# Kernel tuning notes

Hardware: AMD Instinct MI355X
Metric: run time of the kernel (lower is better)

Reference implementation:

```python
import jax, jax.numpy as jnp
import numpy as np

N = 50000
E = 1600000
IN_DIM = 32
EDGE_DIM = 32
HID = 64
OUT = 32


def setup_inputs() -> dict:
    key = jax.random.key(0)
    ks = jax.random.split(key, 12)
    x = jax.random.normal(ks[0], (N, IN_DIM), dtype=jnp.float32)
    edge_index = jax.random.randint(ks[1], (2, E), 0, N, dtype=jnp.int64)
    edge_attr = jax.random.normal(ks[2], (E, EDGE_DIM), dtype=jnp.float32)
    # MLP params: Linear(64->64), Linear(64->128), Linear(128->64), Linear(64->32)
    def lin(k, fan_in, fan_out):
        lim = 1.0 / np.sqrt(fan_in)
        kw, kb = jax.random.split(k)
        W = jax.random.uniform(kw, (fan_in, fan_out), minval=-lim, maxval=lim, dtype=jnp.float32)
        b = jax.random.uniform(kb, (fan_out,), minval=-lim, maxval=lim, dtype=jnp.float32)
        return W, b
    W1, b1 = lin(ks[3], IN_DIM + EDGE_DIM, HID)
    W2, b2 = lin(ks[4], HID, 2 * HID)
    W3, b3 = lin(ks[5], 2 * HID, HID)
    W4, b4 = lin(ks[6], HID, OUT)
    return {"x": x, "edge_index": edge_index, "edge_attr": edge_attr,
            "W1": W1, "b1": b1, "W2": W2, "b2": b2,
            "W3": W3, "b3": b3, "W4": W4, "b4": b4}


def reference(x, edge_index, edge_attr, W1, b1, W2, b2, W3, b3, W4, b4):
    # PyG MessagePassing (source_to_target): x_i = x[edge_index[1]] (target),
    # messages aggregated (mean) at target nodes edge_index[1].
    dst = edge_index[1]
    x_i = x[dst]                                   # [E, IN_DIM] gather
    m = jnp.concatenate([x_i, edge_attr], axis=-1)  # [E, 64]
    # 4-layer MLP with ReLU (dropout = identity at inference)
    m = jax.nn.relu(m @ W1 + b1)                   # [E, 64]
    m = jax.nn.relu(m @ W2 + b2)                   # [E, 128]
    m = jax.nn.relu(m @ W3 + b3)                   # [E, 64]
    m = jax.nn.relu(m @ W4 + b4)                   # [E, 32]
    # mean scatter to target nodes
    sums = jax.ops.segment_sum(m, dst, num_segments=N)          # [N, 32]
    cnt = jax.ops.segment_sum(jnp.ones((E,), m.dtype), dst, num_segments=N)
    out = sums / jnp.maximum(cnt, 1.0)[:, None]
    return out
```

## Files before the change

kernel.cpp:

```cpp
#include <hip/hip_runtime.h>
#include <hip/hip_bf16.h>

typedef __attribute__((ext_vector_type(8))) unsigned short u16x8;
typedef __attribute__((ext_vector_type(8))) __bf16 bf16x8;
typedef __attribute__((ext_vector_type(4))) float f32x4;

__device__ __forceinline__ unsigned pack_bf2(float lo, float hi) {
  unsigned a = __float_as_uint(lo) + 0x8000u;
  unsigned b = __float_as_uint(hi) + 0x8000u;
  return __builtin_amdgcn_perm(b, a, 0x07060302);
}

__device__ __forceinline__ unsigned short f2bf(float f) {
  unsigned u = __float_as_uint(f);
  return (unsigned short)((u + 0x7fffu + ((u >> 16) & 1u)) >> 16);
}

__device__ __forceinline__ int aswz(int row, int feat, int stride) {
  return row * stride + (((feat >> 3) ^ (row & 7)) << 4) + (feat & 7) * 2;
}

__global__ void prep_weights(const float* __restrict__ W1, const float* __restrict__ W2,
                             const float* __restrict__ W3, const float* __restrict__ W4,
                             unsigned short* __restrict__ wt) {
  int i = blockIdx.x * 256 + threadIdx.x;
  if (i >= 22528) return;
  float v; int n, k, K, base;
  if (i < 4096)       { n = i >> 6, k = i & 63;  K = 64;  base = 0;     v = W1[k * 64 + n]; }
  else if (i < 12288) { int j = i - 4096;  n = j >> 6, k = j & 63;  K = 64;  base = 4096;  v = W2[k * 128 + n]; }
  else if (i < 20480) { int j = i - 12288; n = j >> 7, k = j & 127; K = 128; base = 12288; v = W3[k * 64 + n]; }
  else                { int j = i - 20480; n = j >> 6, k = j & 63;  K = 64;  base = 20480; v = W4[k * 32 + n]; }
  int o = base + n * K + ((((k >> 3) ^ (n & 7)) << 3) + (k & 7));
  wt[o] = f2bf(v);
}

__global__ void hist_kernel(const int* __restrict__ ei, int* __restrict__ histI, int E) {
  int e = blockIdx.x * 256 + threadIdx.x;
  if (e < E) atomicAdd(&histI[ei[E + e]], 1);
}

__global__ void scan_blocks(const int* __restrict__ histI, int* __restrict__ row_start,
                            int* __restrict__ blockSums, int N) {
  __shared__ int wsum[4];
  const int lane = threadIdx.x & 63, w = threadIdx.x >> 6;
  const int i0 = blockIdx.x * 2048 + threadIdx.x * 8;
  int v[8];
#pragma unroll
  for (int j = 0; j < 8; ++j) { int i = i0 + j; v[j] = (i < N) ? histI[i] : 0; }
  int s = 0;
#pragma unroll
  for (int j = 0; j < 8; ++j) { int t = v[j]; v[j] = s; s += t; }
  int ss = s;
#pragma unroll
  for (int d = 1; d < 64; d <<= 1) { int t = __shfl_up(ss, d, 64); if (lane >= d) ss += t; }
  if (lane == 63) wsum[w] = ss;
  __syncthreads();
  int wOff = 0;
#pragma unroll
  for (int k = 0; k < 4; ++k) if (k < w) wOff += wsum[k];
  const int tOff = wOff + (ss - s);
#pragma unroll
  for (int j = 0; j < 8; ++j) { int i = i0 + j; if (i < N) row_start[i] = tOff + v[j]; }
  if (threadIdx.x == 255) blockSums[blockIdx.x] = wOff + ss;
}

__global__ void scan_tops(int* __restrict__ blockSums, int nb) {
  const int lane = threadIdx.x;
  int v = (lane < nb) ? blockSums[lane] : 0;
  int s = v;
#pragma unroll
  for (int d = 1; d < 64; d <<= 1) { int t = __shfl_up(s, d, 64); if (lane >= d) s += t; }
  if (lane < nb) blockSums[lane] = s - v;
}

__global__ void scan_add(int* __restrict__ row_start, const int* __restrict__ blockSums, int N) {
  int i = blockIdx.x * 256 + threadIdx.x;
  if (i < N) row_start[i] += blockSums[i >> 11];
}

__global__ void fill_kernel(const int* __restrict__ ei, const int* __restrict__ row_start,
                            int* __restrict__ wcnt, int2* __restrict__ edlist, int E) {
  int e = blockIdx.x * 256 + threadIdx.x;
  if (e >= E) return;
  int d = ei[E + e];
  int slot = atomicAdd(&wcnt[d], 1);
  edlist[row_start[d] + slot] = make_int2(e, d);
}

template <int MT, int KS, int SS, int DS>
__device__ __forceinline__ void mlp_layer(const unsigned char* src, unsigned char* dst,
                                          const unsigned char* wl, const float* biasL, int lane) {
  const int edge = lane & 15, g = lane >> 4;
  asm volatile("s_waitcnt lgkmcnt(0)" ::: "memory");
  u16x8 bfrag[KS];
#pragma unroll
  for (int ks = 0; ks < KS; ++ks)
    bfrag[ks] = *(const u16x8*)(src + aswz(edge, ks * 32 + g * 8, SS));
#pragma unroll
  for (int mt = 0; mt < MT; ++mt) {
    const int n = mt * 16 + edge;
    u16x8 af[KS];
#pragma unroll
    for (int ks = 0; ks < KS; ++ks)
      af[ks] = *(const u16x8*)(wl + n * (KS * 64) + (((ks * 4 + g) ^ (edge & 7)) << 4));
    const float4 bv = *(const float4*)(biasL + mt * 16 + g * 4);
    f32x4 acc = {bv.x, bv.y, bv.z, bv.w};
    __builtin_amdgcn_s_setprio(1);
#pragma unroll
    for (int ks = 0; ks < KS; ++ks)
      acc = __builtin_amdgcn_mfma_f32_16x16x32_bf16(
          __builtin_bit_cast(bf16x8, af[ks]), __builtin_bit_cast(bf16x8, bfrag[ks]),
          acc, 0, 0, 0);
    __builtin_amdgcn_s_setprio(0);
    const int fb = mt * 16 + g * 4;
    uint2 q;
    q.x = pack_bf2(fmaxf(acc[0], 0.f), fmaxf(acc[1], 0.f));
    q.y = pack_bf2(fmaxf(acc[2], 0.f), fmaxf(acc[3], 0.f));
    *(uint2*)(dst + aswz(edge, fb, DS)) = q;
  }
}

__device__ __forceinline__ void load_tile(int ebase, int E, const int2* __restrict__ edlist,
                                          const float* __restrict__ x, const float* __restrict__ ea,
                                          int lane, float4& xa, float4& xb, float4& ya, float4& yb,
                                          int& dstA) {
  const int el = ebase + (lane >> 2);
  const int part = lane & 3;
  xa = make_float4(0.f, 0.f, 0.f, 0.f); xb = xa; ya = xa; yb = xa;
  if (el < E) {
    const int2 ed = edlist[el];
    const float4* xp = (const float4*)(x + (size_t)ed.y * 32 + part * 8);
    xa = xp[0]; xb = xp[1];
    const float4* ep = (const float4*)(ea + (size_t)ed.x * 32 + part * 8);
    ya = ep[0]; yb = ep[1];
  }
  const int pos = ebase + (lane & 15);
  dstA = (pos < E) ? edlist[pos].y : -1;
}

#define BIAS_OFF   45056
#define ACT_OFF    46208

__global__ __launch_bounds__(1024, 4)
void gnn_main(const float* __restrict__ x, const int2* __restrict__ edlist,
              const float* __restrict__ ea, const unsigned short* __restrict__ wt,
              const float* __restrict__ b1, const float* __restrict__ b2,
              const float* __restrict__ b3, const float* __restrict__ b4,
              float* __restrict__ out, int E, int numTiles) {
  __shared__ __align__(16) unsigned char lds[ACT_OFF + 16 * 6144];
  {
    const u16x8* gw = (const u16x8*)wt;
    u16x8* lw = (u16x8*)lds;
    for (int i = threadIdx.x; i < 2816; i += 1024) lw[i] = gw[i];
    float* biasW = (float*)(lds + BIAS_OFF);
    for (int i = threadIdx.x; i < 288; i += 1024) {
      float v;
      if (i < 64) v = b1[i];
      else if (i < 192) v = b2[i - 64];
      else if (i < 256) v = b3[i - 192];
      else v = b4[i - 256];
      biasW[i] = v;
    }
  }
  __syncthreads();

  const int lane = threadIdx.x & 63, wid = threadIdx.x >> 6;
  const int edge = lane & 15, g = lane >> 4;
  const float* biasLds = (const float*)(lds + BIAS_OFF);
  unsigned char* buf0 = lds + ACT_OFF + wid * 6144;
  unsigned char* buf1 = buf0 + 4096;
  const unsigned char* wl1 = lds;
  const unsigned char* wl2 = lds + 8192;
  const unsigned char* wl3 = lds + 24576;
  const unsigned char* wl4 = lds + 40960;

  const int wgl = blockIdx.x * 16 + wid;
  const int wstride = gridDim.x * 16;

  float4 xa, xb, ya, yb; int dstA = -1;
  if (wgl < numTiles) load_tile(wgl * 16, E, edlist, x, ea, lane, xa, xb, ya, yb, dstA);

  for (int tile = wgl; tile < numTiles; tile += wstride) {
    uint4 hx, he;
    hx.x = pack_bf2(xa.x, xa.y); hx.y = pack_bf2(xa.z, xa.w);
    hx.z = pack_bf2(xb.x, xb.y); hx.w = pack_bf2(xb.z, xb.w);
    he.x = pack_bf2(ya.x, ya.y); he.y = pack_bf2(ya.z, ya.w);
    he.z = pack_bf2(yb.x, yb.y); he.w = pack_bf2(yb.z, yb.w);
    const int e2 = lane >> 2, part = lane & 3;
    *(uint4*)(buf0 + aswz(e2, part * 8, 256)) = hx;
    *(uint4*)(buf0 + aswz(e2, 32 + part * 8, 256)) = he;

    const int curDst = dstA;

    const int nt = tile + wstride;
    float4 nxa, nxb, nya, nyb; int ndst = -1;
    if (nt < numTiles) load_tile(nt * 16, E, edlist, x, ea, lane, nxa, nxb, nya, nyb, ndst);
    else { nxa = make_float4(0,0,0,0); nxb = nxa; nya = nxa; nyb = nxa; }

    mlp_layer<4, 2, 256, 128>(buf0, buf1, wl1, biasLds + 0,   lane);
    mlp_layer<8, 2, 128, 256>(buf1, buf0, wl2, biasLds + 64,  lane);
    mlp_layer<4, 4, 256, 128>(buf0, buf1, wl3, biasLds + 192, lane);

    asm volatile("s_waitcnt lgkmcnt(0)" ::: "memory");
    u16x8 bf4[2];
#pragma unroll
    for (int ks = 0; ks < 2; ++ks)
      bf4[ks] = *(const u16x8*)(buf1 + aswz(edge, ks * 32 + g * 8, 128));
    float vals[8];
#pragma unroll
    for (int mt = 0; mt < 2; ++mt) {
      const int n = mt * 16 + edge;
      u16x8 af[2];
#pragma unroll
      for (int ks = 0; ks < 2; ++ks)
        af[ks] = *(const u16x8*)(wl4 + n * 128 + (((ks * 4 + g) ^ (edge & 7)) << 4));
      const float4 bv = *(const float4*)(biasLds + 256 + mt * 16 + g * 4);
      f32x4 acc = {bv.x, bv.y, bv.z, bv.w};
      __builtin_amdgcn_s_setprio(1);
#pragma unroll
      for (int ks = 0; ks < 2; ++ks)
        acc = __builtin_amdgcn_mfma_f32_16x16x32_bf16(
            __builtin_bit_cast(bf16x8, af[ks]), __builtin_bit_cast(bf16x8, bf4[ks]),
            acc, 0, 0, 0);
      __builtin_amdgcn_s_setprio(0);
#pragma unroll
      for (int r = 0; r < 4; ++r) vals[mt * 4 + r] = fmaxf(acc[r], 0.f);
    }

    const int li = edge;
    const int prev = __shfl_up(curDst, 1, 16);
    const bool is_head = (li == 0) || (prev != curDst);
    const unsigned long long hb = __ballot(is_head);
    const unsigned gm = (unsigned)((hb >> (g * 16)) & 0xFFFFu);
    const unsigned below = gm & ((1u << li) | ((1u << li) - 1u));
    const int dist = li - (31 - __clz(below));
#pragma unroll
    for (int d = 1; d < 16; d <<= 1) {
#pragma unroll
      for (int t = 0; t < 8; ++t) {
        const float tv = __shfl_up(vals[t], d, 16);
        if (dist >= d) vals[t] += tv;
      }
    }
    const bool is_end = (li == 15) || ((gm >> (li + 1)) & 1u);
    if (is_end && curDst >= 0) {
      float* op = out + (size_t)curDst * 32 + g * 4;
#pragma unroll
      for (int t = 0; t < 4; ++t) unsafeAtomicAdd(op + t, vals[t]);
#pragma unroll
      for (int t = 0; t < 4; ++t) unsafeAtomicAdd(op + 16 + t, vals[4 + t]);
    }

    xa = nxa; xb = nxb; ya = nya; yb = nyb; dstA = ndst;
  }
}

__global__ void div_kernel(float* __restrict__ out, const int* __restrict__ histI, int total) {
  int i = blockIdx.x * 256 + threadIdx.x;
  if (i < total) out[i] = out[i] / fmaxf((float)histI[i >> 5], 1.0f);
}

extern "C" void kernel_launch(void* const* d_in, const int* in_sizes, int n_in,
                              void* d_out, int out_size, void* d_ws, size_t ws_size,
                              hipStream_t stream) {
  const float* x  = (const float*)d_in[0];
  const int*   ei = (const int*)d_in[1];
  const float* ea = (const float*)d_in[2];
  const float* W1 = (const float*)d_in[3];
  const float* b1 = (const float*)d_in[4];
  const float* W2 = (const float*)d_in[5];
  const float* b2 = (const float*)d_in[6];
  const float* W3 = (const float*)d_in[7];
  const float* b3 = (const float*)d_in[8];
  const float* W4 = (const float*)d_in[9];
  const float* b4 = (const float*)d_in[10];
  const int N = in_sizes[0] / 32;
  const int E = in_sizes[1] / 2;
  float* out = (float*)d_out;

  char* ws = (char*)d_ws;
  size_t off = 0;
  auto alloc = [&](size_t bytes) { size_t o = off; off += (bytes + 255) & ~(size_t)255; return o; };
  int* histI      = (int*)(ws + alloc((size_t)N * 4));
  int* wcnt       = (int*)(ws + alloc((size_t)N * 4));
  int* row_start  = (int*)(ws + alloc((size_t)(N + 1) * 4));
  int* blockSums  = (int*)(ws + alloc(64 * 4));
  int2* edlist    = (int2*)(ws + alloc((size_t)E * 8));
  unsigned short* wt = (unsigned short*)(ws + alloc(22528 * 2));

  hipMemsetAsync(d_out, 0, (size_t)out_size * sizeof(float), stream);
  hipMemsetAsync(histI, 0, (size_t)N * 4, stream);
  hipMemsetAsync(wcnt, 0, (size_t)N * 4, stream);

  prep_weights<<<(22528 + 255) / 256, 256, 0, stream>>>(W1, W2, W3, W4, wt);
  hist_kernel<<<(E + 255) / 256, 256, 0, stream>>>(ei, histI, E);
  const int nb = (N + 2047) / 2048;
  scan_blocks<<<nb, 256, 0, stream>>>(histI, row_start, blockSums, N);
  scan_tops<<<1, 64, 0, stream>>>(blockSums, nb);
  scan_add<<<(N + 255) / 256, 256, 0, stream>>>(row_start, blockSums, N);
  fill_kernel<<<(E + 255) / 256, 256, 0, stream>>>(ei, row_start, wcnt, edlist, E);

  const int numTiles = (E + 15) / 16;
  gnn_main<<<256, 1024, 0, stream>>>(x, edlist, ea, wt, b1, b2, b3, b4, out, E, numTiles);
  const int total = N * 32;
  div_kernel<<<(total + 255) / 256, 256, 0, stream>>>(out, histI, total);
}
```

Baseline: 334.1 us.

## Fuse CSR build into one grid-barrier kernel and use atomic-free node-partitioned mean

Replaces the chain of prep, histogram, multi-stage scan and fill kernels (plus memsets and the divide kernel) with a single persistent kernel that uses software grid barriers. The main kernel now splits work by node ranges found through binary search on row_start, so each destination is owned by one wavefront. Segment sums carry across tiles and are written once, already divided by the count, instead of using atomic adds followed by a separate division pass. This cuts launch overhead and atomic traffic, but depends on all 256 blocks being co-resident for the barrier and adds more complex carry logic. The main grid also grows from 256 to 512 blocks.

```diff
diff --git a/kernel.cpp b/kernel.cpp
--- a/kernel.cpp
+++ b/kernel.cpp
@@ -4,6 +4,8 @@
 typedef __attribute__((ext_vector_type(8))) unsigned short u16x8;
 typedef __attribute__((ext_vector_type(8))) __bf16 bf16x8;
 typedef __attribute__((ext_vector_type(4))) float f32x4;
+
+#define CSR_NB 256
 
 __device__ __forceinline__ unsigned pack_bf2(float lo, float hi) {
   unsigned a = __float_as_uint(lo) + 0x8000u;
@@ -20,71 +22,107 @@
   return row * stride + (((feat >> 3) ^ (row & 7)) << 4) + (feat & 7) * 2;
 }
 
-__global__ void prep_weights(const float* __restrict__ W1, const float* __restrict__ W2,
-                             const float* __restrict__ W3, const float* __restrict__ W4,
-                             unsigned short* __restrict__ wt) {
-  int i = blockIdx.x * 256 + threadIdx.x;
-  if (i >= 22528) return;
-  float v; int n, k, K, base;
-  if (i < 4096)       { n = i >> 6, k = i & 63;  K = 64;  base = 0;     v = W1[k * 64 + n]; }
-  else if (i < 12288) { int j = i - 4096;  n = j >> 6, k = j & 63;  K = 64;  base = 4096;  v = W2[k * 128 + n]; }
-  else if (i < 20480) { int j = i - 12288; n = j >> 7, k = j & 127; K = 128; base = 12288; v = W3[k * 64 + n]; }
-  else                { int j = i - 20480; n = j >> 6, k = j & 63;  K = 64;  base = 20480; v = W4[k * 32 + n]; }
-  int o = base + n * K + ((((k >> 3) ^ (n & 7)) << 3) + (k & 7));
-  wt[o] = f2bf(v);
-}
-
-__global__ void hist_kernel(const int* __restrict__ ei, int* __restrict__ histI, int E) {
-  int e = blockIdx.x * 256 + threadIdx.x;
-  if (e < E) atomicAdd(&histI[ei[E + e]], 1);
-}
-
-__global__ void scan_blocks(const int* __restrict__ histI, int* __restrict__ row_start,
-                            int* __restrict__ blockSums, int N) {
+__device__ __forceinline__ void gbar(int* bar, int id) {
+  __threadfence();
+  __syncthreads();
+  if (threadIdx.x == 0) {
+    __hip_atomic_fetch_add(&bar[id], 1, __ATOMIC_ACQ_REL, __HIP_MEMORY_SCOPE_AGENT);
+    while (__hip_atomic_load(&bar[id], __ATOMIC_ACQUIRE, __HIP_MEMORY_SCOPE_AGENT) < CSR_NB)
+      __builtin_amdgcn_s_sleep(2);
+  }
+  __syncthreads();
+}
+
+__global__ __launch_bounds__(256)
+void csr_build(const float* __restrict__ W1, const float* __restrict__ W2,
+               const float* __restrict__ W3, const float* __restrict__ W4,
+               unsigned short* __restrict__ wt, const int* __restrict__ ei,
+               int* __restrict__ histI, int* __restrict__ row_start,
+               int* __restrict__ blockSums, int* __restrict__ wcnt,
+               int2* __restrict__ edlist, float* __restrict__ out,
+               int* __restrict__ bar, int E, int N) {
+  const int tid = blockIdx.x * 256 + threadIdx.x;
+  const int lane = threadIdx.x & 63, w = threadIdx.x >> 6;
+  const int NTH = CSR_NB * 256;
   __shared__ int wsum[4];
-  const int lane = threadIdx.x & 63, w = threadIdx.x >> 6;
-  const int i0 = blockIdx.x * 2048 + threadIdx.x * 8;
-  int v[8];
-#pragma unroll
-  for (int j = 0; j < 8; ++j) { int i = i0 + j; v[j] = (i < N) ? histI[i] : 0; }
-  int s = 0;
-#pragma unroll
-  for (int j = 0; j < 8; ++j) { int t = v[j]; v[j] = s; s += t; }
-  int ss = s;
-#pragma unroll
-  for (int d = 1; d < 64; d <<= 1) { int t = __shfl_up(ss, d, 64); if (lane >= d) ss += t; }
-  if (lane == 63) wsum[w] = ss;
+
+  if (tid < 22528) {
+    float v; int n, k, K, base;
+    if (tid < 4096)       { n = tid >> 6, k = tid & 63;  K = 64;  base = 0;     v = W1[k * 64 + n]; }
+    else if (tid < 12288) { int j = tid - 4096;  n = j >> 6, k = j & 63;  K = 64;  base = 4096;  v = W2[k * 128 + n]; }
+    else if (tid < 20480) { int j = tid - 12288; n = j >> 7, k = j & 127; K = 128; base = 12288; v = W3[k * 64 + n]; }
+    else                  { int j = tid - 20480; n = j >> 6, k = j & 63;  K = 64;  base = 20480; v = W4[k * 32 + n]; }
+    int o = base + n * K + ((((k >> 3) ^ (n & 7)) << 3) + (k & 7));
+    wt[o] = f2bf(v);
+  }
+  const int Ntot4 = N * 8;
+  for (int i = tid; i < Ntot4; i += NTH)
+    ((float4*)out)[i] = make_float4(0.f, 0.f, 0.f, 0.f);
+  for (int e0 = tid * 4; e0 < E; e0 += NTH * 4) {
+    if (e0 + 3 < E) {
+      const int4 d4 = *(const int4*)(ei + E + e0);
+      atomicAdd(&histI[d4.x], 1); atomicAdd(&histI[d4.y], 1);
+      atomicAdd(&histI[d4.z], 1); atomicAdd(&histI[d4.w], 1);
+    } else {
+      for (int e = e0; e < E; ++e) atomicAdd(&histI[ei[E + e]], 1);
+    }
+  }
+  gbar(bar, 0);
+
+  const int i = tid;
+  const int v = (i < N) ? histI[i] : 0;
+  int s = v;
+#pragma unroll
+  for (int d = 1; d < 64; d <<= 1) { int t = __shfl_up(s, d, 64); if (lane >= d) s += t; }
+  if (lane == 63) wsum[w] = s;
   __syncthreads();
   int wOff = 0;
 #pragma unroll
   for (int k = 0; k < 4; ++k) if (k < w) wOff += wsum[k];
-  const int tOff = wOff + (ss - s);
-#pragma unroll
-  for (int j = 0; j < 8; ++j) { int i = i0 + j; if (i < N) row_start[i] = tOff + v[j]; }
-  if (threadIdx.x == 255) blockSums[blockIdx.x] = wOff + ss;
-}
-
-__global__ void scan_tops(int* __restrict__ blockSums, int nb) {
-  const int lane = threadIdx.x;
-  int v = (lane < nb) ? blockSums[lane] : 0;
-  int s = v;
-#pragma unroll
-  for (int d = 1; d < 64; d <<= 1) { int t = __shfl_up(s, d, 64); if (lane >= d) s += t; }
-  if (lane < nb) blockSums[lane] = s - v;
-}
-
-__global__ void scan_add(int* __restrict__ row_start, const int* __restrict__ blockSums, int N) {
-  int i = blockIdx.x * 256 + threadIdx.x;
-  if (i < N) row_start[i] += blockSums[i >> 11];
-}
-
-__global__ void fill_kernel(const int* __restrict__ ei, const int* __restrict__ row_start,
-                            int* __restrict__ wcnt, int2* __restrict__ edlist, int E) {
-  int e = blockIdx.x * 256 + threadIdx.x;
-  if (e >= E) return;
-  int d = ei[E + e];
-  int slot = atomicAdd(&wcnt[d], 1);
-  edlist[row_start[d] + slot] = make_int2(e, d);
+  const int lexcl = wOff + (s - v);
+  if (threadIdx.x == 0) {
+    int bt = wsum[0] + wsum[1] + wsum[2] + wsum[3];
+    blockSums[blockIdx.x] = bt;
+  }
+  gbar(bar, 1);
+
+  if (blockIdx.x == 0 && threadIdx.x < 64) {
+    int run = 0;
+    for (int c = 0; c < 4; ++c) {
+      const int idx = c * 64 + lane;
+      const int bv = blockSums[idx];
+      int bs = bv;
+#pragma unroll
+      for (int d = 1; d < 64; d <<= 1) { int t = __shfl_up(bs, d, 64); if (lane >= d) bs += t; }
+      const int ctot = __shfl(bs, 63, 64);
+      blockSums[idx] = run + bs - bv;
+      run += ctot;
+    }
+    if (lane == 0) row_start[N] = E;
+  }
+  gbar(bar, 2);
+
+  if (i < N) row_start[i] = blockSums[blockIdx.x] + lexcl;
+  gbar(bar, 3);
+
+  for (int e0 = tid * 4; e0 < E; e0 += NTH * 4) {
+    if (e0 + 3 < E) {
+      const int4 d4 = *(const int4*)(ei + E + e0);
+      const int dv[4] = {d4.x, d4.y, d4.z, d4.w};
+#pragma unroll
+      for (int j = 0; j < 4; ++j) {
+        const int d = dv[j];
+        const int slot = atomicAdd(&wcnt[d], 1);
+        edlist[row_start[d] + slot] = make_int2(e0 + j, d);
+      }
+    } else {
+      for (int e = e0; e < E; ++e) {
+        const int d = ei[E + e];
+        const int slot = atomicAdd(&wcnt[d], 1);
+        edlist[row_start[d] + slot] = make_int2(e, d);
+      }
+    }
+  }
 }
 
 template <int MT, int KS, int SS, int DS>
@@ -120,33 +158,40 @@
   }
 }
 
-__device__ __forceinline__ void load_tile(int ebase, int E, const int2* __restrict__ edlist,
+__device__ __forceinline__ void load_tile(int pbase, int pend, const int2* __restrict__ edlist,
                                           const float* __restrict__ x, const float* __restrict__ ea,
                                           int lane, float4& xa, float4& xb, float4& ya, float4& yb,
                                           int& dstA) {
-  const int el = ebase + (lane >> 2);
+  const int el = pbase + (lane >> 2);
   const int part = lane & 3;
   xa = make_float4(0.f, 0.f, 0.f, 0.f); xb = xa; ya = xa; yb = xa;
-  if (el < E) {
+  if (el < pend) {
     const int2 ed = edlist[el];
     const float4* xp = (const float4*)(x + (size_t)ed.y * 32 + part * 8);
     xa = xp[0]; xb = xp[1];
     const float4* ep = (const float4*)(ea + (size_t)ed.x * 32 + part * 8);
     ya = ep[0]; yb = ep[1];
   }
-  const int pos = ebase + (lane & 15);
-  dstA = (pos < E) ? edlist[pos].y : -1;
-}
-
-#define BIAS_OFF   45056
-#define ACT_OFF    46208
+  const int pos = pbase + (lane & 15);
+  dstA = (pos < pend) ? edlist[pos].y : -1;
+}
+
+__device__ __forceinline__ int lbound(const int* __restrict__ rs, int N, long tgt) {
+  int lo = 0, hi = N;
+  while (lo < hi) { int mid = (lo + hi) >> 1; if ((long)rs[mid] < tgt) lo = mid + 1; else hi = mid; }
+  return lo;
+}
+
+#define BIAS_OFF 45056
+#define ACT_OFF  46208
 
 __global__ __launch_bounds__(1024, 4)
 void gnn_main(const float* __restrict__ x, const int2* __restrict__ edlist,
               const float* __restrict__ ea, const unsigned short* __restrict__ wt,
+              const int* __restrict__ row_start,
               const float* __restrict__ b1, const float* __restrict__ b2,
               const float* __restrict__ b3, const float* __restrict__ b4,
-              float* __restrict__ out, int E, int numTiles) {
+              float* __restrict__ out, int E, int N) {
   __shared__ __align__(16) unsigned char lds[ACT_OFF + 16 * 6144];
   {
     const u16x8* gw = (const u16x8*)wt;
@@ -165,7 +210,7 @@
   __syncthreads();
 
   const int lane = threadIdx.x & 63, wid = threadIdx.x >> 6;
-  const int edge = lane & 15, g = lane >> 4;
+  const int li = lane & 15, g = lane >> 4;
   const float* biasLds = (const float*)(lds + BIAS_OFF);
   unsigned char* buf0 = lds + ACT_OFF + wid * 6144;
   unsigned char* buf1 = buf0 + 4096;
@@ -175,12 +220,21 @@
   const unsigned char* wl4 = lds + 40960;
 
   const int wgl = blockIdx.x * 16 + wid;
-  const int wstride = gridDim.x * 16;
+  const int W = gridDim.x * 16;
+  const int n0 = lbound(row_start, N, (long)wgl * E / W);
+  const int n1 = lbound(row_start, N, (long)(wgl + 1) * E / W);
+  const int pstart = row_start[n0];
+  const int pend = row_start[n1];
 
   float4 xa, xb, ya, yb; int dstA = -1;
-  if (wgl < numTiles) load_tile(wgl * 16, E, edlist, x, ea, lane, xa, xb, ya, yb, dstA);
-
-  for (int tile = wgl; tile < numTiles; tile += wstride) {
+  if (pstart < pend) load_tile(pstart, pend, edlist, x, ea, lane, xa, xb, ya, yb, dstA);
+
+  float carry[8];
+#pragma unroll
+  for (int t = 0; t < 8; ++t) carry[t] = 0.f;
+  int cDst = -1, cCnt = 0;
+
+  for (int pbase = pstart; pbase < pend; pbase += 16) {
     uint4 hx, he;
     hx.x = pack_bf2(xa.x, xa.y); hx.y = pack_bf2(xa.z, xa.w);
     hx.z = pack_bf2(xb.x, xb.y); hx.w = pack_bf2(xb.z, xb.w);
@@ -192,9 +246,9 @@
 
     const int curDst = dstA;
 
-    const int nt = tile + wstride;
-    float4 nxa, nxb, nya, nyb; int ndst = -1;
-    if (nt < numTiles) load_tile(nt * 16, E, edlist, x, ea, lane, nxa, nxb, nya, nyb, ndst);
+    const int np = pbase + 16;
+    float4 nxa, nxb, nya, nyb; int nd = -1;
+    if (np < pend) load_tile(np, pend, edlist, x, ea, lane, nxa, nxb, nya, nyb, nd);
     else { nxa = make_float4(0,0,0,0); nxb = nxa; nya = nxa; nyb = nxa; }
 
     mlp_layer<4, 2, 256, 128>(buf0, buf1, wl1, biasLds + 0,   lane);
@@ -205,15 +259,15 @@
     u16x8 bf4[2];
 #pragma unroll
     for (int ks = 0; ks < 2; ++ks)
-      bf4[ks] = *(const u16x8*)(buf1 + aswz(edge, ks * 32 + g * 8, 128));
+      bf4[ks] = *(const u16x8*)(buf1 + aswz(li, ks * 32 + g * 8, 128));
     float vals[8];
 #pragma unroll
     for (int mt = 0; mt < 2; ++mt) {
-      const int n = mt * 16 + edge;
+      const int n = mt * 16 + li;
       u16x8 af[2];
 #pragma unroll
       for (int ks = 0; ks < 2; ++ks)
-        af[ks] = *(const u16x8*)(wl4 + n * 128 + (((ks * 4 + g) ^ (edge & 7)) << 4));
+        af[ks] = *(const u16x8*)(wl4 + n * 128 + (((ks * 4 + g) ^ (li & 7)) << 4));
       const float4 bv = *(const float4*)(biasLds + 256 + mt * 16 + g * 4);
       f32x4 acc = {bv.x, bv.y, bv.z, bv.w};
       __builtin_amdgcn_s_setprio(1);
@@ -227,37 +281,97 @@
       for (int r = 0; r < 4; ++r) vals[mt * 4 + r] = fmaxf(acc[r], 0.f);
     }
 
-    const int li = edge;
-    const int prev = __shfl_up(curDst, 1, 16);
-    const bool is_head = (li == 0) || (prev != curDst);
-    const unsigned long long hb = __ballot(is_head);
-    const unsigned gm = (unsigned)((hb >> (g * 16)) & 0xFFFFu);
-    const unsigned below = gm & ((1u << li) | ((1u << li) - 1u));
-    const int dist = li - (31 - __clz(below));
-#pragma unroll
-    for (int d = 1; d < 16; d <<= 1) {
+    if (__all(curDst == cDst)) {
+#pragma unroll
+      for (int t = 0; t < 8; ++t) carry[t] += vals[t];
+      cCnt += 16;
+    } else {
+      const int prev = __shfl_up(curDst, 1, 16);
+      const bool is_head = (li == 0) || (prev != curDst);
+      const unsigned long long hb = __ballot(is_head);
+      const unsigned gm = (unsigned)((hb >> (g * 16)) & 0xFFFFu);
+      const unsigned below = gm & ((1u << li) | ((1u << li) - 1u));
+      const int dist = li - (31 - __clz(below));
+
+      float ctot[8];
 #pragma unroll
       for (int t = 0; t < 8; ++t) {
-        const float tv = __shfl_up(vals[t], d, 16);
-        if (dist >= d) vals[t] += tv;
-      }
-    }
-    const bool is_end = (li == 15) || ((gm >> (li + 1)) & 1u);
-    if (is_end && curDst >= 0) {
-      float* op = out + (size_t)curDst * 32 + g * 4;
-#pragma unroll
-      for (int t = 0; t < 4; ++t) unsafeAtomicAdd(op + t, vals[t]);
-#pragma unroll
-      for (int t = 0; t < 4; ++t) unsafeAtomicAdd(op + 16 + t, vals[4 + t]);
-    }
-
-    xa = nxa; xb = nxb; ya = nya; yb = nyb; dstA = ndst;
-  }
-}
-
-__global__ void div_kernel(float* __restrict__ out, const int* __restrict__ histI, int total) {
-  int i = blockIdx.x * 256 + threadIdx.x;
-  if (i < total) out[i] = out[i] / fmaxf((float)histI[i >> 5], 1.0f);
+        float c = carry[t];
+#pragma unroll
+        for (int d = 1; d < 16; d <<= 1) c += __shfl_xor(c, d, 16);
+        ctot[t] = c;
+      }
+
+      const int dst0 = __shfl(curDst, lane & 48, 64);
+      if (cDst >= 0 && dst0 != cDst && li == 0) {
+        const float inv = 1.0f / (float)cCnt;
+        float4 o0 = {ctot[0] * inv, ctot[1] * inv, ctot[2] * inv, ctot[3] * inv};
+        float4 o1 = {ctot[4] * inv, ctot[5] * inv, ctot[6] * inv, ctot[7] * inv};
+        *(float4*)(out + (size_t)cDst * 32 + g * 4) = o0;
+        *(float4*)(out + (size_t)cDst * 32 + 16 + g * 4) = o1;
+      }
+
+#pragma unroll
+      for (int d = 1; d < 16; d <<= 1) {
+#pragma unroll
+        for (int t = 0; t < 8; ++t) {
+          const float tv = __shfl_up(vals[t], d, 16);
+          if (dist >= d) vals[t] += tv;
+        }
+      }
+
+      const int ndst0 = __shfl(nd, lane & 48, 64);
+      const bool is_end = (li == 15) || ((gm >> (li + 1)) & 1u);
+      const bool complete = (li < 15) || (curDst != ndst0);
+      const bool firstAdd = (dist == li) && (curDst == cDst) && (cDst >= 0);
+      if (is_end && curDst >= 0 && complete) {
+        const int cnt = dist + 1 + (firstAdd ? cCnt : 0);
+        const float inv = 1.0f / (float)cnt;
+        float tot[8];
+#pragma unroll
+        for (int t = 0; t < 8; ++t) tot[t] = (vals[t] + (firstAdd ? ctot[t] : 0.f)) * inv;
+        float4 o0 = {tot[0], tot[1], tot[2], tot[3]};
+        float4 o1 = {tot[4], tot[5], tot[6], tot[7]};
+        *(float4*)(out + (size_t)curDst * 32 + g * 4) = o0;
+        *(float4*)(out + (size_t)curDst * 32 + 16 + g * 4) = o1;
+      }
+
+      const int dst15 = __shfl(curDst, lane | 15, 64);
+      const int d15 = __shfl(dist, lane | 15, 64);
+      const bool inc15 = (dst15 >= 0) && (dst15 == ndst0);
+      if (inc15) {
+#pragma unroll
+        for (int t = 0; t < 8; ++t)
+          carry[t] = (li == 15) ? (vals[t] + (firstAdd ? ctot[t] : 0.f)) : 0.f;
+        cCnt = d15 + 1 + ((d15 == 15 && dst15 == cDst) ? cCnt : 0);
+        cDst = dst15;
+      } else {
+#pragma unroll
+        for (int t = 0; t < 8; ++t) carry[t] = 0.f;
+        cCnt = 0; cDst = -1;
+      }
+    }
+
+    xa = nxa; xb = nxb; ya = nya; yb = nyb; dstA = nd;
+  }
+
+  if (cDst >= 0) {
+    float ctot[8];
+#pragma unroll
+    for (int t = 0; t < 8; ++t) {
+      float c = carry[t];
+#pragma unroll
+      for (int d = 1; d < 16; d <<= 1) c += __shfl_xor(c, d, 16);
+      ctot[t] = c;
+    }
+    if (li == 0) {
+      const float inv = 1.0f / (float)cCnt;
+      float4 o0 = {ctot[0] * inv, ctot[1] * inv, ctot[2] * inv, ctot[3] * inv};
+      float4 o1 = {ctot[4] * inv, ctot[5] * inv, ctot[6] * inv, ctot[7] * inv};
+      *(float4*)(out + (size_t)cDst * 32 + g * 4) = o0;
+      *(float4*)(out + (size_t)cDst * 32 + 16 + g * 4) = o1;
+    }
+  }
 }
 
 extern "C" void kernel_launch(void* const* d_in, const int* in_sizes, int n_in,
@@ -281,27 +395,21 @@
   char* ws = (char*)d_ws;
   size_t off = 0;
   auto alloc = [&](size_t bytes) { size_t o = off; off += (bytes + 255) & ~(size_t)255; return o; };
-  int* histI      = (int*)(ws + alloc((size_t)N * 4));
-  int* wcnt       = (int*)(ws + alloc((size_t)N * 4));
+  size_t bar_off  = alloc(256);
+  size_t hist_off = alloc((size_t)N * 4);
+  size_t wcnt_off = alloc((size_t)N * 4);
+  int* bar        = (int*)(ws + bar_off);
+  int* histI      = (int*)(ws + hist_off);
+  int* wcnt       = (int*)(ws + wcnt_off);
   int* row_start  = (int*)(ws + alloc((size_t)(N + 1) * 4));
-  int* blockSums  = (int*)(ws + alloc(64 * 4));
+  int* blockSums  = (int*)(ws + alloc(256 * 4));
   int2* edlist    = (int2*)(ws + alloc((size_t)E * 8));
   unsigned short* wt = (unsigned short*)(ws + alloc(22528 * 2));
 
-  hipMemsetAsync(d_out, 0, (size_t)out_size * sizeof(float), stream);
-  hipMemsetAsync(histI, 0, (size_t)N * 4, stream);
-  hipMemsetAsync(wcnt, 0, (size_t)N * 4, stream);
-
-  prep_weights<<<(22528 + 255) / 256, 256, 0, stream>>>(W1, W2, W3, W4, wt);
-  hist_kernel<<<(E + 255) / 256, 256, 0, stream>>>(ei, histI, E);
-  const int nb = (N + 2047) / 2048;
-  scan_blocks<<<nb, 256, 0, stream>>>(histI, row_start, blockSums, N);
-  scan_tops<<<1, 64, 0, stream>>>(blockSums, nb);
-  scan_add<<<(N + 255) / 256, 256, 0, stream>>>(row_start, blockSums, N);
-  fill_kernel<<<(E + 255) / 256, 256, 0, stream>>>(ei, row_start, wcnt, edlist, E);
-
-  const int numTiles = (E + 15) / 16;
-  gnn_main<<<256, 1024, 0, stream>>>(x, edlist, ea, wt, b1, b2, b3, b4, out, E, numTiles);
-  const int total = N * 32;
-  div_kernel<<<(total + 255) / 256, 256, 0, stream>>>(out, histI, total);
-}
+  hipMemsetAsync(ws, 0, wcnt_off + (size_t)N * 4, stream);
+
+  csr_build<<<CSR_NB, 256, 0, stream>>>(W1, W2, W3, W4, wt, ei, histI, row_start,
+                                        blockSums, wcnt, edlist, out, bar, E, N);
+  gnn_main<<<512, 1024, 0, stream>>>(x, edlist, ea, wt, row_start,
+                                     b1, b2, b3, b4, out, E, N);
+}
```

Result: slower. 450.4 us (+34.8%).

## Fuse preprocessing launches, partition atomics by XCD, fold mean division into scatter

Applied to the files above, without the earlier changes.

Merges weight prep with the histogram, and folds the top-level scan and scan-add into the fill kernel through a per-block serial prefix. The output zeroing also moves into the fill kernel, and the separate division kernel is removed by scaling each segment sum by the reciprocal of its destination count before the atomic add. Histogram and fill atomics are split by destination range per block-index modulo 8, aiming to keep atomics local to one XCD's L2 (assumes blocks are dispatched round-robin across XCDs). In exchange, every block re-reads the edge indices and filters them (8x the index reads), and the main kernel gathers one extra count per edge.

```diff
diff --git a/kernel.cpp b/kernel.cpp
--- a/kernel.cpp
+++ b/kernel.cpp
@@ -20,23 +20,33 @@
   return row * stride + (((feat >> 3) ^ (row & 7)) << 4) + (feat & 7) * 2;
 }
 
-__global__ void prep_weights(const float* __restrict__ W1, const float* __restrict__ W2,
-                             const float* __restrict__ W3, const float* __restrict__ W4,
-                             unsigned short* __restrict__ wt) {
-  int i = blockIdx.x * 256 + threadIdx.x;
-  if (i >= 22528) return;
-  float v; int n, k, K, base;
-  if (i < 4096)       { n = i >> 6, k = i & 63;  K = 64;  base = 0;     v = W1[k * 64 + n]; }
-  else if (i < 12288) { int j = i - 4096;  n = j >> 6, k = j & 63;  K = 64;  base = 4096;  v = W2[k * 128 + n]; }
-  else if (i < 20480) { int j = i - 12288; n = j >> 7, k = j & 127; K = 128; base = 12288; v = W3[k * 64 + n]; }
-  else                { int j = i - 20480; n = j >> 6, k = j & 63;  K = 64;  base = 20480; v = W4[k * 32 + n]; }
-  int o = base + n * K + ((((k >> 3) ^ (n & 7)) << 3) + (k & 7));
-  wt[o] = f2bf(v);
-}
-
-__global__ void hist_kernel(const int* __restrict__ ei, int* __restrict__ histI, int E) {
-  int e = blockIdx.x * 256 + threadIdx.x;
-  if (e < E) atomicAdd(&histI[ei[E + e]], 1);
+__global__ __launch_bounds__(256)
+void prep_hist(const float* __restrict__ W1, const float* __restrict__ W2,
+               const float* __restrict__ W3, const float* __restrict__ W4,
+               unsigned short* __restrict__ wt,
+               const int* __restrict__ ei, int* __restrict__ histI, int E, int N) {
+  const int tid = threadIdx.x;
+  const int i = blockIdx.x * 256 + tid;
+  if (i < 22528) {
+    float v; int n, k, K, base;
+    if (i < 4096)       { n = i >> 6, k = i & 63;  K = 64;  base = 0;     v = W1[k * 64 + n]; }
+    else if (i < 12288) { int j = i - 4096;  n = j >> 6, k = j & 63;  K = 64;  base = 4096;  v = W2[k * 128 + n]; }
+    else if (i < 20480) { int j = i - 12288; n = j >> 7, k = j & 127; K = 128; base = 12288; v = W3[k * 64 + n]; }
+    else                { int j = i - 20480; n = j >> 6, k = j & 63;  K = 64;  base = 20480; v = W4[k * 32 + n]; }
+    int o = base + n * K + ((((k >> 3) ^ (n & 7)) << 3) + (k & 7));
+    wt[o] = f2bf(v);
+  }
+  const int xcd = blockIdx.x & 7, kblk = blockIdx.x >> 3;
+  const int nchunks = gridDim.x >> 3;
+  const int chunk = (E + nchunks - 1) / nchunks;
+  const int eBeg = kblk * chunk;
+  const int eEnd = min(eBeg + chunk, E);
+  const int dLo = (int)((long)xcd * N / 8);
+  const int dHi = (int)((long)(xcd + 1) * N / 8);
+  for (int e = eBeg + tid; e < eEnd; e += 256) {
+    const int d = ei[E + e];
+    if (d >= dLo && d < dHi) atomicAdd(&histI[d], 1);
+  }
 }
 
 __global__ void scan_blocks(const int* __restrict__ histI, int* __restrict__ row_start,
@@ -64,27 +74,36 @@
   if (threadIdx.x == 255) blockSums[blockIdx.x] = wOff + ss;
 }
 
-__global__ void scan_tops(int* __restrict__ blockSums, int nb) {
-  const int lane = threadIdx.x;
-  int v = (lane < nb) ? blockSums[lane] : 0;
-  int s = v;
-#pragma unroll
-  for (int d = 1; d < 64; d <<= 1) { int t = __shfl_up(s, d, 64); if (lane >= d) s += t; }
-  if (lane < nb) blockSums[lane] = s - v;
-}
-
-__global__ void scan_add(int* __restrict__ row_start, const int* __restrict__ blockSums, int N) {
-  int i = blockIdx.x * 256 + threadIdx.x;
-  if (i < N) row_start[i] += blockSums[i >> 11];
-}
-
-__global__ void fill_kernel(const int* __restrict__ ei, const int* __restrict__ row_start,
-                            int* __restrict__ wcnt, int2* __restrict__ edlist, int E) {
-  int e = blockIdx.x * 256 + threadIdx.x;
-  if (e >= E) return;
-  int d = ei[E + e];
-  int slot = atomicAdd(&wcnt[d], 1);
-  edlist[row_start[d] + slot] = make_int2(e, d);
+__global__ __launch_bounds__(256)
+void fill_kernel(const int* __restrict__ ei, const int* __restrict__ row_start,
+                 const int* __restrict__ blockSums, int* __restrict__ wcnt,
+                 int2* __restrict__ edlist, float* __restrict__ out,
+                 int E, int N, int nb) {
+  __shared__ int spre[32];
+  if (threadIdx.x == 0) {
+    int acc = 0;
+    for (int k = 0; k < nb; ++k) { spre[k] = acc; acc += blockSums[k]; }
+  }
+  __syncthreads();
+  const int tid = threadIdx.x;
+  const int Ntot4 = N * 8;
+  for (int i = blockIdx.x * 256 + tid; i < Ntot4; i += gridDim.x * 256)
+    ((float4*)out)[i] = make_float4(0.f, 0.f, 0.f, 0.f);
+
+  const int xcd = blockIdx.x & 7, kblk = blockIdx.x >> 3;
+  const int nchunks = gridDim.x >> 3;
+  const int chunk = (E + nchunks - 1) / nchunks;
+  const int eBeg = kblk * chunk;
+  const int eEnd = min(eBeg + chunk, E);
+  const int dLo = (int)((long)xcd * N / 8);
+  const int dHi = (int)((long)(xcd + 1) * N / 8);
+  for (int e = eBeg + tid; e < eEnd; e += 256) {
+    const int d = ei[E + e];
+    if (d >= dLo && d < dHi) {
+      const int slot = atomicAdd(&wcnt[d], 1);
+      edlist[row_start[d] + spre[d >> 11] + slot] = make_int2(e, d);
+    }
+  }
 }
 
 template <int MT, int KS, int SS, int DS>
@@ -122,8 +141,9 @@
 
 __device__ __forceinline__ void load_tile(int ebase, int E, const int2* __restrict__ edlist,
                                           const float* __restrict__ x, const float* __restrict__ ea,
+                                          const int* __restrict__ histI,
                                           int lane, float4& xa, float4& xb, float4& ya, float4& yb,
-                                          int& dstA) {
+                                          int& dstA, int& cntA) {
   const int el = ebase + (lane >> 2);
   const int part = lane & 3;
   xa = make_float4(0.f, 0.f, 0.f, 0.f); xb = xa; ya = xa; yb = xa;
@@ -135,15 +155,20 @@
     ya = ep[0]; yb = ep[1];
   }
   const int pos = ebase + (lane & 15);
-  dstA = (pos < E) ? edlist[pos].y : -1;
-}
-
-#define BIAS_OFF   45056
-#define ACT_OFF    46208
+  dstA = -1; cntA = 1;
+  if (pos < E) {
+    dstA = edlist[pos].y;
+    cntA = histI[dstA];
+  }
+}
+
+#define BIAS_OFF 45056
+#define ACT_OFF  46208
 
 __global__ __launch_bounds__(1024, 4)
 void gnn_main(const float* __restrict__ x, const int2* __restrict__ edlist,
               const float* __restrict__ ea, const unsigned short* __restrict__ wt,
+              const int* __restrict__ histI,
               const float* __restrict__ b1, const float* __restrict__ b2,
               const float* __restrict__ b3, const float* __restrict__ b4,
               float* __restrict__ out, int E, int numTiles) {
@@ -165,7 +190,7 @@
   __syncthreads();
 
   const int lane = threadIdx.x & 63, wid = threadIdx.x >> 6;
-  const int edge = lane & 15, g = lane >> 4;
+  const int li = lane & 15, g = lane >> 4;
   const float* biasLds = (const float*)(lds + BIAS_OFF);
   unsigned char* buf0 = lds + ACT_OFF + wid * 6144;
   unsigned char* buf1 = buf0 + 4096;
@@ -177,8 +202,8 @@
   const int wgl = blockIdx.x * 16 + wid;
   const int wstride = gridDim.x * 16;
 
-  float4 xa, xb, ya, yb; int dstA = -1;
-  if (wgl < numTiles) load_tile(wgl * 16, E, edlist, x, ea, lane, xa, xb, ya, yb, dstA);
+  float4 xa, xb, ya, yb; int dstA = -1, cntA = 1;
+  if (wgl < numTiles) load_tile(wgl * 16, E, edlist, x, ea, histI, lane, xa, xb, ya, yb, dstA, cntA);
 
   for (int tile = wgl; tile < numTiles; tile += wstride) {
     uint4 hx, he;
@@ -190,11 +215,11 @@
     *(uint4*)(buf0 + aswz(e2, part * 8, 256)) = hx;
     *(uint4*)(buf0 + aswz(e2, 32 + part * 8, 256)) = he;
 
-    const int curDst = dstA;
+    const int curDst = dstA, curCnt = cntA;
 
     const int nt = tile + wstride;
-    float4 nxa, nxb, nya, nyb; int ndst = -1;
-    if (nt < numTiles) load_tile(nt * 16, E, edlist, x, ea, lane, nxa, nxb, nya, nyb, ndst);
+    float4 nxa, nxb, nya, nyb; int nd = -1, nc = 1;
+    if (nt < numTiles) load_tile(nt * 16, E, edlist, x, ea, histI, lane, nxa, nxb, nya, nyb, nd, nc);
     else { nxa = make_float4(0,0,0,0); nxb = nxa; nya = nxa; nyb = nxa; }
 
     mlp_layer<4, 2, 256, 128>(buf0, buf1, wl1, biasLds + 0,   lane);
@@ -205,15 +230,15 @@
     u16x8 bf4[2];
 #pragma unroll
     for (int ks = 0; ks < 2; ++ks)
-      bf4[ks] = *(const u16x8*)(buf1 + aswz(edge, ks * 32 + g * 8, 128));
+      bf4[ks] = *(const u16x8*)(buf1 + aswz(li, ks * 32 + g * 8, 128));
     float vals[8];
 #pragma unroll
     for (int mt = 0; mt < 2; ++mt) {
-      const int n = mt * 16 + edge;
+      const int n = mt * 16 + li;
       u16x8 af[2];
 #pragma unroll
       for (int ks = 0; ks < 2; ++ks)
-        af[ks] = *(const u16x8*)(wl4 + n * 128 + (((ks * 4 + g) ^ (edge & 7)) << 4));
+        af[ks] = *(const u16x8*)(wl4 + n * 128 + (((ks * 4 + g) ^ (li & 7)) << 4));
       const float4 bv = *(const float4*)(biasLds + 256 + mt * 16 + g * 4);
       f32x4 acc = {bv.x, bv.y, bv.z, bv.w};
       __builtin_amdgcn_s_setprio(1);
@@ -227,7 +252,6 @@
       for (int r = 0; r < 4; ++r) vals[mt * 4 + r] = fmaxf(acc[r], 0.f);
     }
 
-    const int li = edge;
     const int prev = __shfl_up(curDst, 1, 16);
     const bool is_head = (li == 0) || (prev != curDst);
     const unsigned long long hb = __ballot(is_head);
@@ -244,20 +268,16 @@
     }
     const bool is_end = (li == 15) || ((gm >> (li + 1)) & 1u);
     if (is_end && curDst >= 0) {
+      const float inv = 1.0f / (float)curCnt;
       float* op = out + (size_t)curDst * 32 + g * 4;
 #pragma unroll
-      for (int t = 0; t < 4; ++t) unsafeAtomicAdd(op + t, vals[t]);
-#pragma unroll
-      for (int t = 0; t < 4; ++t) unsafeAtomicAdd(op + 16 + t, vals[4 + t]);
-    }
-
-    xa = nxa; xb = nxb; ya = nya; yb = nyb; dstA = ndst;
-  }
-}
-
-__global__ void div_kernel(float* __restrict__ out, const int* __restrict__ histI, int total) {
-  int i = blockIdx.x * 256 + threadIdx.x;
-  if (i < total) out[i] = out[i] / fmaxf((float)histI[i >> 5], 1.0f);
+      for (int t = 0; t < 4; ++t) unsafeAtomicAdd(op + t, vals[t] * inv);
+#pragma unroll
+      for (int t = 0; t < 4; ++t) unsafeAtomicAdd(op + 16 + t, vals[4 + t] * inv);
+    }
+
+    xa = nxa; xb = nxb; ya = nya; yb = nyb; dstA = nd; cntA = nc;
+  }
 }
 
 extern "C" void kernel_launch(void* const* d_in, const int* in_sizes, int n_in,
@@ -281,27 +301,22 @@
   char* ws = (char*)d_ws;
   size_t off = 0;
   auto alloc = [&](size_t bytes) { size_t o = off; off += (bytes + 255) & ~(size_t)255; return o; };
-  int* histI      = (int*)(ws + alloc((size_t)N * 4));
-  int* wcnt       = (int*)(ws + alloc((size_t)N * 4));
+  size_t hist_off = alloc((size_t)N * 4);
+  size_t wcnt_off = alloc((size_t)N * 4);
+  int* histI      = (int*)(ws + hist_off);
+  int* wcnt       = (int*)(ws + wcnt_off);
   int* row_start  = (int*)(ws + alloc((size_t)(N + 1) * 4));
-  int* blockSums  = (int*)(ws + alloc(64 * 4));
+  int* blockSums  = (int*)(ws + alloc(256 * 4));
   int2* edlist    = (int2*)(ws + alloc((size_t)E * 8));
   unsigned short* wt = (unsigned short*)(ws + alloc(22528 * 2));
 
-  hipMemsetAsync(d_out, 0, (size_t)out_size * sizeof(float), stream);
-  hipMemsetAsync(histI, 0, (size_t)N * 4, stream);
-  hipMemsetAsync(wcnt, 0, (size_t)N * 4, stream);
-
-  prep_weights<<<(22528 + 255) / 256, 256, 0, stream>>>(W1, W2, W3, W4, wt);
-  hist_kernel<<<(E + 255) / 256, 256, 0, stream>>>(ei, histI, E);
+  hipMemsetAsync(ws + hist_off, 0, (wcnt_off - hist_off) + (size_t)N * 4, stream);
+
+  prep_hist<<<2048, 256, 0, stream>>>(W1, W2, W3, W4, wt, ei, histI, E, N);
   const int nb = (N + 2047) / 2048;
   scan_blocks<<<nb, 256, 0, stream>>>(histI, row_start, blockSums, N);
-  scan_tops<<<1, 64, 0, stream>>>(blockSums, nb);
-  scan_add<<<(N + 255) / 256, 256, 0, stream>>>(row_start, blockSums, N);
-  fill_kernel<<<(E + 255) / 256, 256, 0, stream>>>(ei, row_start, wcnt, edlist, E);
-
+  fill_kernel<<<2048, 256, 0, stream>>>(ei, row_start, blockSums, wcnt, edlist, out, E, N, nb);
   const int numTiles = (E + 15) / 16;
-  gnn_main<<<256, 1024, 0, stream>>>(x, edlist, ea, wt, b1, b2, b3, b4, out, E, numTiles);
-  const int total = N * 32;
-  div_kernel<<<(total + 255) / 256, 256, 0, stream>>>(out, histI, total);
-}
+  gnn_main<<<256, 1024, 0, stream>>>(x, edlist, ea, wt, histI,
+                                     b1, b2, b3, b4, out, E, numTiles);
+}
```

Measured after the change: 314.5 us. 1.06x faster.
